# Optimization experiments

Hardware: AMD Instinct MI355X
Metric: run time of the kernel (lower is better)

Reference implementation:

```python
import jax, jax.numpy as jnp
import numpy as np
from jax import lax

B, H, S, D = 4, 12, 4096, 64
TILE = 128


def setup_inputs() -> dict:
    key = jax.random.key(0)
    kq, kk, kv = jax.random.split(key, 3)
    query = jax.random.normal(kq, (B, H, S, D), dtype=jnp.float32)
    key_t = jax.random.normal(kk, (B, H, S, D), dtype=jnp.float32)
    value = jax.random.normal(kv, (B, H, S, D), dtype=jnp.float32)
    return {"query": query, "key": key_t, "value": value}


def _flash_tiled(query, key, value):
    b, h, s, d = query.shape
    scale = d ** (-0.5)
    nq = s // TILE
    nk = s // TILE
    # q tiles: [b, h, nq, TILE, d]; kv tiles scanned along leading axis
    q = query.reshape(b, h, nq, TILE, d)
    k = key.reshape(b, h, nk, TILE, d).transpose(2, 0, 1, 3, 4)    # [nk,b,h,TILE,d]
    v = value.reshape(b, h, nk, TILE, d).transpose(2, 0, 1, 3, 4)  # [nk,b,h,TILE,d]

    out0 = jnp.zeros((b, h, nq, TILE, d), dtype=query.dtype)
    m0 = jnp.full((b, h, nq, TILE, 1), -jnp.inf, dtype=query.dtype)
    s0 = jnp.zeros((b, h, nq, TILE, 1), dtype=query.dtype)

    def step(carry, kv_tiles):
        out, m, ssum = carry
        k_tile, v_tile = kv_tiles
        # scores: [b,h,nq,TILE_q,TILE_k]
        scores = jnp.einsum('bhntd,bhsd->bhnts', q, k_tile) * scale
        cur_max = jnp.max(scores, axis=-1, keepdims=True)
        new_max = jnp.maximum(m, cur_max)
        old_scale = jnp.exp(m - new_max)
        cur_scale = jnp.exp(cur_max - new_max)  # extra factor, faithful to source
        cur_exp = jnp.exp(scores - new_max)
        out = out * old_scale + cur_scale * jnp.einsum('bhnts,bhsd->bhntd', cur_exp, v_tile)
        ssum = ssum * old_scale + cur_scale * jnp.sum(cur_exp, axis=-1, keepdims=True)
        return (out, new_max, ssum), None

    (out, _, ssum), _ = lax.scan(step, (out0, m0, s0), (k, v))
    return (out / ssum).reshape(b, h, s, d)


def reference(query, key, value):
    return _flash_tiled(query, key, value)
```

## Files before the change

kernel.cpp:

```cpp
#include <hip/hip_runtime.h>
#include <hip/hip_bf16.h>


#define S_LEN 4096
#define HD    64
#define QTILE 128
#define KTILE 128
#define NKT   32

#define KSTR  72
#define VSTR  136
#define VT_OFF (128 * KSTR)
#define SMEM_U16 (VT_OFF + HD * VSTR)
#define OSTR  68

typedef __attribute__((ext_vector_type(8))) short bf16x8;
typedef __attribute__((ext_vector_type(4))) short bf16x4;
typedef __attribute__((ext_vector_type(4))) float f32x4;

__device__ __forceinline__ unsigned int pk2(float f0, float f1) {
    unsigned int u0 = __builtin_bit_cast(unsigned int, f0);
    unsigned int u1 = __builtin_bit_cast(unsigned int, f1);
    u0 += 0x7FFFu + ((u0 >> 16) & 1u);
    u1 += 0x7FFFu + ((u1 >> 16) & 1u);
    return __builtin_amdgcn_perm(u1, u0, 0x07060302u);
}
__device__ __forceinline__ unsigned int pkt(float f0, float f1) {
    return __builtin_amdgcn_perm(__builtin_bit_cast(unsigned int, f1),
                                 __builtin_bit_cast(unsigned int, f0),
                                 0x07060302u);
}
__device__ __forceinline__ float e2(float x) {
#if __has_builtin(__builtin_amdgcn_exp2f)
    return __builtin_amdgcn_exp2f(x);
#else
    return __expf(x * 0.6931471805599453f);
#endif
}
__device__ __forceinline__ float rcp(float x) {
#if __has_builtin(__builtin_amdgcn_rcpf)
    return __builtin_amdgcn_rcpf(x);
#else
    return 1.0f / x;
#endif
}

__global__ __launch_bounds__(256, 3)
void fattn_kernel(const float* __restrict__ Q,
                  const float* __restrict__ K,
                  const float* __restrict__ V,
                  float* __restrict__ O) {
    __shared__ __align__(16) unsigned short smem[SMEM_U16];

    const int t    = threadIdx.x;
    const int wave = t >> 6;
    const int lane = t & 63;
    const int m    = lane & 15;
    const int quad = lane >> 4;

    const int qblk = blockIdx.x;
    const int head = blockIdx.y;
    const size_t hbase = (size_t)head * S_LEN * HD;

    unsigned short* const Kl = smem;
    unsigned short* const Vt = smem + VT_OFF;

    bf16x8 qf[2][2];
    #pragma unroll
    for (int rt = 0; rt < 2; ++rt) {
        const float* qp = Q + hbase +
            (size_t)(qblk * QTILE + wave * 32 + rt * 16 + m) * HD + quad * 8;
        #pragma unroll
        for (int kd = 0; kd < 2; ++kd) {
            float4 a = *(const float4*)(qp + kd * 32);
            float4 b = *(const float4*)(qp + kd * 32 + 4);
            union { unsigned int u[4]; bf16x8 v; } cv;
            const float s = 0.1803368801111f;
            cv.u[0] = pk2(a.x * s, a.y * s);
            cv.u[1] = pk2(a.z * s, a.w * s);
            cv.u[2] = pk2(b.x * s, b.y * s);
            cv.u[3] = pk2(b.z * s, b.w * s);
            qf[rt][kd] = cv.v;
        }
    }

    bf16x8 ones;
    {
        unsigned int oo = (m == 0) ? 0x3F803F80u : 0u;
        union { unsigned int u[4]; bf16x8 v; } cv;
        cv.u[0] = oo; cv.u[1] = oo; cv.u[2] = oo; cv.u[3] = oo;
        ones = cv.v;
    }

    f32x4 oacc[4][2];
    f32x4 lacc[2];
    float mrow[2] = {-INFINITY, -INFINITY};
    #pragma unroll
    for (int dt = 0; dt < 4; ++dt)
        #pragma unroll
        for (int rt = 0; rt < 2; ++rt) oacc[dt][rt] = (f32x4){0.f,0.f,0.f,0.f};
    lacc[0] = (f32x4){0.f,0.f,0.f,0.f};
    lacc[1] = (f32x4){0.f,0.f,0.f,0.f};

    const int r0k = t >> 3;
    const int c0k = (t & 7) * 8;
    const int chk = ((t & 7) + ((t >> 3) & 7)) & 7;
    const int vp_ = t & 63;
    const int vd0 = (t >> 6) * 16;
    unsigned short* const kwb = &Kl[r0k * KSTR + chk * 8];
    unsigned short* const vwb = &Vt[vd0 * VSTR + 2 * vp_];
    const unsigned short* const kb0 = &Kl[m * KSTR + (((quad + m) & 7) << 3)];
    const unsigned short* const kb1 = &Kl[m * KSTR + (((4 + quad + m) & 7) << 3)];
    const unsigned short* const vrb = &Vt[m * VSTR + quad * 4];

    float4 va[2][4];
    {
        const float* vp = V + hbase + (size_t)(2 * vp_) * HD + vd0;
        #pragma unroll
        for (int e = 0; e < 2; ++e)
            #pragma unroll
            for (int j = 0; j < 4; ++j)
                va[e][j] = *(const float4*)(vp + e * HD + j * 4);
    }

    for (int kt = 0; kt < NKT; ++kt) {
        __syncthreads();

        #pragma unroll
        for (int d = 0; d < 16; ++d) {
            float f0 = ((const float*)&va[0][0])[d];
            float f1 = ((const float*)&va[1][0])[d];
            *(unsigned int*)(vwb + d * VSTR) = pk2(f0, f1);
        }
        {
            const float* kp = K + hbase + (size_t)(kt * KTILE + r0k) * HD + c0k;
            #pragma unroll
            for (int i = 0; i < 4; ++i) {
                float4 a = *(const float4*)(kp + i * 32 * HD);
                float4 b = *(const float4*)(kp + i * 32 * HD + 4);
                union { unsigned int u[4]; bf16x8 v; } cv;
                cv.u[0] = pk2(a.x, a.y); cv.u[1] = pk2(a.z, a.w);
                cv.u[2] = pk2(b.x, b.y); cv.u[3] = pk2(b.z, b.w);
                *(bf16x8*)(kwb + i * 32 * KSTR) = cv.v;
            }
        }
        __syncthreads();

        {
            int nk = (kt + 1 < NKT) ? kt + 1 : 0;
            const float* vp = V + hbase + (size_t)(nk * KTILE + 2 * vp_) * HD + vd0;
            #pragma unroll
            for (int e = 0; e < 2; ++e)
                #pragma unroll
                for (int j = 0; j < 4; ++j)
                    va[e][j] = *(const float4*)(vp + e * HD + j * 4);
        }

        f32x4 sacc[8][2];
        #pragma unroll
        for (int k8 = 0; k8 < 8; ++k8)
            #pragma unroll
            for (int rt = 0; rt < 2; ++rt) sacc[k8][rt] = (f32x4){0.f,0.f,0.f,0.f};

        #pragma unroll
        for (int k8 = 0; k8 < 8; ++k8) {
            bf16x8 kf0 = *(const bf16x8*)(kb0 + k8 * 16 * KSTR);
            bf16x8 kf1 = *(const bf16x8*)(kb1 + k8 * 16 * KSTR);
            sacc[k8][0] = __builtin_amdgcn_mfma_f32_16x16x32_bf16(
                kf0, qf[0][0], sacc[k8][0], 0, 0, 0);
            sacc[k8][1] = __builtin_amdgcn_mfma_f32_16x16x32_bf16(
                kf0, qf[1][0], sacc[k8][1], 0, 0, 0);
            sacc[k8][0] = __builtin_amdgcn_mfma_f32_16x16x32_bf16(
                kf1, qf[0][1], sacc[k8][0], 0, 0, 0);
            sacc[k8][1] = __builtin_amdgcn_mfma_f32_16x16x32_bf16(
                kf1, qf[1][1], sacc[k8][1], 0, 0, 0);
        }

        unsigned int pkv[8][2][2];
        #pragma unroll
        for (int rt = 0; rt < 2; ++rt) {
            float cm = fmaxf(fmaxf(sacc[0][rt][0], sacc[0][rt][1]),
                             fmaxf(sacc[0][rt][2], sacc[0][rt][3]));
            #pragma unroll
            for (int k8 = 1; k8 < 8; ++k8) {
                float a = fmaxf(sacc[k8][rt][0], sacc[k8][rt][1]);
                float b = fmaxf(sacc[k8][rt][2], sacc[k8][rt][3]);
                cm = fmaxf(cm, fmaxf(a, b));
            }
            cm = fmaxf(cm, __shfl_xor(cm, 16, 64));
            cm = fmaxf(cm, __shfl_xor(cm, 32, 64));

            float mo = mrow[rt];
            float mn = fmaxf(mo, cm);
            float bias = cm - mn - mn;
            mrow[rt] = mn;

            if (__any(cm > mo)) {
                float osc = e2(mo - mn);
                #pragma unroll
                for (int dt = 0; dt < 4; ++dt) {
                    oacc[dt][rt][0] *= osc; oacc[dt][rt][1] *= osc;
                    oacc[dt][rt][2] *= osc; oacc[dt][rt][3] *= osc;
                }
                lacc[rt][0] *= osc;
            }

            #pragma unroll
            for (int k8 = 0; k8 < 8; ++k8) {
                float p0 = e2(sacc[k8][rt][0] + bias);
                float p1 = e2(sacc[k8][rt][1] + bias);
                float p2 = e2(sacc[k8][rt][2] + bias);
                float p3 = e2(sacc[k8][rt][3] + bias);
                pkv[k8][rt][0] = pkt(p0, p1);
                pkv[k8][rt][1] = pkt(p2, p3);
            }
        }

        #pragma unroll
        for (int kc = 0; kc < 4; ++kc) {
            bf16x8 pf[2];
            #pragma unroll
            for (int rt = 0; rt < 2; ++rt) {
                union { unsigned int u[4]; bf16x8 v; } cv;
                cv.u[0] = pkv[2 * kc][rt][0];
                cv.u[1] = pkv[2 * kc][rt][1];
                cv.u[2] = pkv[2 * kc + 1][rt][0];
                cv.u[3] = pkv[2 * kc + 1][rt][1];
                pf[rt] = cv.v;
            }
            #pragma unroll
            for (int dt = 0; dt < 4; ++dt) {
                union { struct { bf16x4 lo, hi; } s; bf16x8 v; } uf;
                uf.s.lo = *(const bf16x4*)(vrb + dt * 16 * VSTR + kc * 32);
                uf.s.hi = *(const bf16x4*)(vrb + dt * 16 * VSTR + kc * 32 + 16);
                oacc[dt][0] = __builtin_amdgcn_mfma_f32_16x16x32_bf16(
                    uf.v, pf[0], oacc[dt][0], 0, 0, 0);
                oacc[dt][1] = __builtin_amdgcn_mfma_f32_16x16x32_bf16(
                    uf.v, pf[1], oacc[dt][1], 0, 0, 0);
            }
            lacc[0] = __builtin_amdgcn_mfma_f32_16x16x32_bf16(
                ones, pf[0], lacc[0], 0, 0, 0);
            lacc[1] = __builtin_amdgcn_mfma_f32_16x16x32_bf16(
                ones, pf[1], lacc[1], 0, 0, 0);
        }
    }

    __syncthreads();
    float* Ol = (float*)smem;
    #pragma unroll
    for (int rt = 0; rt < 2; ++rt) {
        #pragma unroll
        for (int dt = 0; dt < 4; ++dt)
            #pragma unroll
            for (int r = 0; r < 4; ++r)
                Ol[(wave * 32 + rt * 16 + m) * OSTR + dt * 16 + quad * 4 + r] =
                    oacc[dt][rt][r];
        if (quad == 0)
            Ol[(wave * 32 + rt * 16 + m) * OSTR + 64] = lacc[rt][0];
    }
    __syncthreads();
    const size_t obase = hbase + (size_t)(qblk * QTILE) * HD;
    #pragma unroll
    for (int s = 0; s < 8; ++s) {
        int row = s * 16 + (t >> 4);
        int col = (t & 15) * 4;
        float inv = rcp(Ol[row * OSTR + 64]);
        const float* src = &Ol[row * OSTR + col];
        float4 o;
        o.x = src[0] * inv; o.y = src[1] * inv;
        o.z = src[2] * inv; o.w = src[3] * inv;
        *(float4*)&O[obase + (size_t)row * HD + col] = o;
    }
}

extern "C" void kernel_launch(void* const* d_in, const int* in_sizes, int n_in,
                              void* d_out, int out_size, void* d_ws, size_t ws_size,
                              hipStream_t stream) {
    (void)in_sizes; (void)n_in; (void)d_ws; (void)ws_size; (void)out_size;
    const float* Q = (const float*)d_in[0];
    const float* K = (const float*)d_in[1];
    const float* V = (const float*)d_in[2];
    float* O = (float*)d_out;
    dim3 grid(S_LEN / QTILE, 4 * 12);
    fattn_kernel<<<grid, 256, 0, stream>>>(Q, K, V, O);
}
```

Before: 564.9 us.

## Double Q tile to 256 rows with 512-thread blocks and shuffle-based row sums

Each block now handles 256 query rows with 8 waves, so every K/V tile staged in shared memory serves twice as many queries and total K/V global traffic and conversion work halve. The row-sum accumulation moves from an MFMA against a ones vector to a scalar sum with cross-lane shuffles. The rescale of the output accumulator becomes unconditional, dropping the wave vote. The V transpose store is rewritten to one key per thread with 16-bit stores, and the epilogue writes output in two phases through shared memory. Larger blocks and launch bounds of 512,4 raise register pressure and may lower occupancy; the 16-bit LDS stores are narrower.

```diff
diff --git a/kernel.cpp b/kernel.cpp
--- a/kernel.cpp
+++ b/kernel.cpp
@@ -4,7 +4,7 @@
 
 #define S_LEN 4096
 #define HD    64
-#define QTILE 128
+#define QTILE 256
 #define KTILE 128
 #define NKT   32
 
@@ -45,7 +45,7 @@
 #endif
 }
 
-__global__ __launch_bounds__(256, 3)
+__global__ __launch_bounds__(512, 4)
 void fattn_kernel(const float* __restrict__ Q,
                   const float* __restrict__ K,
                   const float* __restrict__ V,
@@ -75,7 +75,7 @@
             float4 a = *(const float4*)(qp + kd * 32);
             float4 b = *(const float4*)(qp + kd * 32 + 4);
             union { unsigned int u[4]; bf16x8 v; } cv;
-            const float s = 0.1803368801111f;
+            const float s = 0.18033688011112042f;
             cv.u[0] = pk2(a.x * s, a.y * s);
             cv.u[1] = pk2(a.z * s, a.w * s);
             cv.u[2] = pk2(b.x * s, b.y * s);
@@ -84,43 +84,30 @@
         }
     }
 
-    bf16x8 ones;
-    {
-        unsigned int oo = (m == 0) ? 0x3F803F80u : 0u;
-        union { unsigned int u[4]; bf16x8 v; } cv;
-        cv.u[0] = oo; cv.u[1] = oo; cv.u[2] = oo; cv.u[3] = oo;
-        ones = cv.v;
-    }
-
     f32x4 oacc[4][2];
-    f32x4 lacc[2];
     float mrow[2] = {-INFINITY, -INFINITY};
+    float lrow[2] = {0.f, 0.f};
     #pragma unroll
     for (int dt = 0; dt < 4; ++dt)
         #pragma unroll
         for (int rt = 0; rt < 2; ++rt) oacc[dt][rt] = (f32x4){0.f,0.f,0.f,0.f};
-    lacc[0] = (f32x4){0.f,0.f,0.f,0.f};
-    lacc[1] = (f32x4){0.f,0.f,0.f,0.f};
 
     const int r0k = t >> 3;
     const int c0k = (t & 7) * 8;
     const int chk = ((t & 7) + ((t >> 3) & 7)) & 7;
-    const int vp_ = t & 63;
-    const int vd0 = (t >> 6) * 16;
+    const int vkey = t & 127;
+    const int vdb  = (t >> 7) * 16;
     unsigned short* const kwb = &Kl[r0k * KSTR + chk * 8];
-    unsigned short* const vwb = &Vt[vd0 * VSTR + 2 * vp_];
+    unsigned short* const vwp = &Vt[vdb * VSTR + vkey];
     const unsigned short* const kb0 = &Kl[m * KSTR + (((quad + m) & 7) << 3)];
     const unsigned short* const kb1 = &Kl[m * KSTR + (((4 + quad + m) & 7) << 3)];
     const unsigned short* const vrb = &Vt[m * VSTR + quad * 4];
 
-    float4 va[2][4];
+    float4 va[4];
     {
-        const float* vp = V + hbase + (size_t)(2 * vp_) * HD + vd0;
-        #pragma unroll
-        for (int e = 0; e < 2; ++e)
-            #pragma unroll
-            for (int j = 0; j < 4; ++j)
-                va[e][j] = *(const float4*)(vp + e * HD + j * 4);
+        const float* vp = V + hbase + (size_t)vkey * HD + vdb;
+        #pragma unroll
+        for (int j = 0; j < 4; ++j) va[j] = *(const float4*)(vp + j * 4);
     }
 
     for (int kt = 0; kt < NKT; ++kt) {
@@ -128,32 +115,29 @@
 
         #pragma unroll
         for (int d = 0; d < 16; ++d) {
-            float f0 = ((const float*)&va[0][0])[d];
-            float f1 = ((const float*)&va[1][0])[d];
-            *(unsigned int*)(vwb + d * VSTR) = pk2(f0, f1);
+            float f = ((const float*)va)[d];
+            unsigned int u = __builtin_bit_cast(unsigned int, f) + 0x8000u;
+            vwp[d * VSTR] = (unsigned short)(u >> 16);
         }
         {
             const float* kp = K + hbase + (size_t)(kt * KTILE + r0k) * HD + c0k;
             #pragma unroll
-            for (int i = 0; i < 4; ++i) {
-                float4 a = *(const float4*)(kp + i * 32 * HD);
-                float4 b = *(const float4*)(kp + i * 32 * HD + 4);
+            for (int i = 0; i < 2; ++i) {
+                float4 a = *(const float4*)(kp + i * 64 * HD);
+                float4 b = *(const float4*)(kp + i * 64 * HD + 4);
                 union { unsigned int u[4]; bf16x8 v; } cv;
                 cv.u[0] = pk2(a.x, a.y); cv.u[1] = pk2(a.z, a.w);
                 cv.u[2] = pk2(b.x, b.y); cv.u[3] = pk2(b.z, b.w);
-                *(bf16x8*)(kwb + i * 32 * KSTR) = cv.v;
+                *(bf16x8*)(kwb + i * 64 * KSTR) = cv.v;
             }
         }
         __syncthreads();
 
         {
             int nk = (kt + 1 < NKT) ? kt + 1 : 0;
-            const float* vp = V + hbase + (size_t)(nk * KTILE + 2 * vp_) * HD + vd0;
-            #pragma unroll
-            for (int e = 0; e < 2; ++e)
-                #pragma unroll
-                for (int j = 0; j < 4; ++j)
-                    va[e][j] = *(const float4*)(vp + e * HD + j * 4);
+            const float* vp = V + hbase + (size_t)(nk * KTILE + vkey) * HD + vdb;
+            #pragma unroll
+            for (int j = 0; j < 4; ++j) va[j] = *(const float4*)(vp + j * 4);
         }
 
         f32x4 sacc[8][2];
@@ -192,28 +176,30 @@
 
             float mo = mrow[rt];
             float mn = fmaxf(mo, cm);
+            float osc = e2(mo - mn);
             float bias = cm - mn - mn;
             mrow[rt] = mn;
 
-            if (__any(cm > mo)) {
-                float osc = e2(mo - mn);
-                #pragma unroll
-                for (int dt = 0; dt < 4; ++dt) {
-                    oacc[dt][rt][0] *= osc; oacc[dt][rt][1] *= osc;
-                    oacc[dt][rt][2] *= osc; oacc[dt][rt][3] *= osc;
-                }
-                lacc[rt][0] *= osc;
-            }
-
+            #pragma unroll
+            for (int dt = 0; dt < 4; ++dt) {
+                oacc[dt][rt][0] *= osc; oacc[dt][rt][1] *= osc;
+                oacc[dt][rt][2] *= osc; oacc[dt][rt][3] *= osc;
+            }
+
+            float rs = 0.f;
             #pragma unroll
             for (int k8 = 0; k8 < 8; ++k8) {
                 float p0 = e2(sacc[k8][rt][0] + bias);
                 float p1 = e2(sacc[k8][rt][1] + bias);
                 float p2 = e2(sacc[k8][rt][2] + bias);
                 float p3 = e2(sacc[k8][rt][3] + bias);
+                rs += (p0 + p1) + (p2 + p3);
                 pkv[k8][rt][0] = pkt(p0, p1);
                 pkv[k8][rt][1] = pkt(p2, p3);
             }
+            rs += __shfl_xor(rs, 16, 64);
+            rs += __shfl_xor(rs, 32, 64);
+            lrow[rt] = lrow[rt] * osc + rs;
         }
 
         #pragma unroll
@@ -238,38 +224,34 @@
                 oacc[dt][1] = __builtin_amdgcn_mfma_f32_16x16x32_bf16(
                     uf.v, pf[1], oacc[dt][1], 0, 0, 0);
             }
-            lacc[0] = __builtin_amdgcn_mfma_f32_16x16x32_bf16(
-                ones, pf[0], lacc[0], 0, 0, 0);
-            lacc[1] = __builtin_amdgcn_mfma_f32_16x16x32_bf16(
-                ones, pf[1], lacc[1], 0, 0, 0);
-        }
-    }
-
-    __syncthreads();
+        }
+    }
+
     float* Ol = (float*)smem;
-    #pragma unroll
-    for (int rt = 0; rt < 2; ++rt) {
-        #pragma unroll
-        for (int dt = 0; dt < 4; ++dt)
-            #pragma unroll
-            for (int r = 0; r < 4; ++r)
-                Ol[(wave * 32 + rt * 16 + m) * OSTR + dt * 16 + quad * 4 + r] =
-                    oacc[dt][rt][r];
-        if (quad == 0)
-            Ol[(wave * 32 + rt * 16 + m) * OSTR + 64] = lacc[rt][0];
-    }
-    __syncthreads();
     const size_t obase = hbase + (size_t)(qblk * QTILE) * HD;
     #pragma unroll
-    for (int s = 0; s < 8; ++s) {
-        int row = s * 16 + (t >> 4);
-        int col = (t & 15) * 4;
-        float inv = rcp(Ol[row * OSTR + 64]);
-        const float* src = &Ol[row * OSTR + col];
-        float4 o;
-        o.x = src[0] * inv; o.y = src[1] * inv;
-        o.z = src[2] * inv; o.w = src[3] * inv;
-        *(float4*)&O[obase + (size_t)row * HD + col] = o;
+    for (int ph = 0; ph < 2; ++ph) {
+        __syncthreads();
+        if ((wave >> 2) == ph) {
+            #pragma unroll
+            for (int rt = 0; rt < 2; ++rt) {
+                float inv = rcp(lrow[rt]);
+                #pragma unroll
+                for (int dt = 0; dt < 4; ++dt)
+                    #pragma unroll
+                    for (int r = 0; r < 4; ++r)
+                        Ol[((wave & 3) * 32 + rt * 16 + m) * OSTR +
+                           dt * 16 + quad * 4 + r] = oacc[dt][rt][r] * inv;
+            }
+        }
+        __syncthreads();
+        #pragma unroll
+        for (int s = 0; s < 4; ++s) {
+            int lr  = s * 32 + (t >> 4);
+            int col = (t & 15) * 4;
+            *(float4*)&O[obase + (size_t)(ph * 128 + lr) * HD + col] =
+                *(const float4*)&Ol[lr * OSTR + col];
+        }
     }
 }
 
@@ -282,5 +264,5 @@
     const float* V = (const float*)d_in[2];
     float* O = (float*)d_out;
     dim3 grid(S_LEN / QTILE, 4 * 12);
-    fattn_kernel<<<grid, 256, 0, stream>>>(Q, K, V, O);
-}
+    fattn_kernel<<<grid, 512, 0, stream>>>(Q, K, V, O);
+}
```

New measurement: 718.3 us. 1.27x slower.
